# Kernel optimization log

Hardware: AMD Instinct MI355X
Metric: run time of the kernel (lower is better)

## Reference

```python
import jax, jax.numpy as jnp
import numpy as np

N, E, G = 50000, 640000, 512
F_NODE, F_EDGE, HID, H, L = 8, 3, 128, 4, 4
C = HID // H


def setup_inputs() -> dict:
    key = jax.random.key(0)
    ks = jax.random.split(key, 24)
    p = lambda k, s: jax.random.normal(k, s, jnp.float32) * 0.1
    return {
        "x": jax.random.normal(ks[0], (N, F_NODE), jnp.float32),
        "edge_attr": jax.random.normal(ks[1], (E, F_EDGE), jnp.float32),
        "edge_index": jax.random.randint(ks[2], (2, E), 0, N, dtype=jnp.int32),
        "batch": jnp.sort(jax.random.randint(ks[3], (N,), 0, G, dtype=jnp.int32)),
        "enc_node_w": p(ks[4], (F_NODE, HID)), "enc_node_b": p(ks[5], (HID,)),
        "enc_edge_w": p(ks[6], (F_EDGE, HID)), "enc_edge_b": p(ks[7], (HID,)),
        "gat_lin_w": p(ks[8], (L, HID, HID)),
        "gat_att_src": p(ks[9], (L, H, C)),
        "gat_att_dst": p(ks[10], (L, H, C)),
        "gat_lin_edge_w": p(ks[11], (L, HID, HID)),
        "gat_att_edge": p(ks[12], (L, H, C)),
        "gat_bias": p(ks[13], (L, HID)),
        "bn_gamma": jnp.ones((L, HID), jnp.float32),
        "bn_beta": jnp.zeros((L, HID), jnp.float32),
        "fc1_w": p(ks[14], (HID, HID)), "fc1_b": p(ks[15], (HID,)),
        "fc2_w": p(ks[16], (HID, HID // 2)), "fc2_b": p(ks[17], (HID // 2,)),
        "fc3_w": p(ks[18], (HID // 2, 1)), "fc3_b": p(ks[19], (1,)),
    }


def _gat(x, src, dst, ea, lin_w, a_src, a_dst, lin_e_w, a_edge, bias):
    # PyG GATConv (concat=True, negative_slope=0.2, edge_dim=HID)
    xp = (x @ lin_w).reshape(N, H, C)                      # [N,H,C]
    s = jnp.einsum('nhc,hc->nh', xp, a_src)                # alpha_src per node
    d = jnp.einsum('nhc,hc->nh', xp, a_dst)                # alpha_dst per node
    ep = (ea @ lin_e_w).reshape(-1, H, C)                  # [Et,H,C]
    e = jnp.einsum('ehc,hc->eh', ep, a_edge)               # alpha_edge per edge
    alpha = jax.nn.leaky_relu(s[src] + d[dst] + e, 0.2)    # [Et,H]
    # segment softmax over incoming edges of each target node
    m = jax.ops.segment_max(alpha, dst, num_segments=N)
    w = jnp.exp(alpha - m[dst])
    z = jax.ops.segment_sum(w, dst, num_segments=N)
    w = w / (z[dst] + 1e-16)
    msg = xp[src] * w[:, :, None]                          # [Et,H,C]
    out = jax.ops.segment_sum(msg, dst, num_segments=N)
    return out.reshape(N, HID) + bias


def reference(x, edge_attr, edge_index, batch,
              enc_node_w, enc_node_b, enc_edge_w, enc_edge_b,
              gat_lin_w, gat_att_src, gat_att_dst, gat_lin_edge_w, gat_att_edge, gat_bias,
              bn_gamma, bn_beta, fc1_w, fc1_b, fc2_w, fc2_b, fc3_w, fc3_b):
    src, dst = edge_index[0], edge_index[1]
    h = x @ enc_node_w + enc_node_b
    ea = edge_attr @ enc_edge_w + enc_edge_b
    # add_self_loops with fill_value='mean': self-loop attr = mean of incoming edge attrs
    deg = jax.ops.segment_sum(jnp.ones((E,), h.dtype), dst, num_segments=N)
    loop_ea = jax.ops.segment_sum(ea, dst, num_segments=N) / jnp.maximum(deg, 1.0)[:, None]
    loop = jnp.arange(N, dtype=src.dtype)
    src_f = jnp.concatenate([src, loop])
    dst_f = jnp.concatenate([dst, loop])
    ea_f = jnp.concatenate([ea, loop_ea], axis=0)
    for i in range(L):
        hn = _gat(h, src_f, dst_f, ea_f, gat_lin_w[i], gat_att_src[i], gat_att_dst[i],
                  gat_lin_edge_w[i], gat_att_edge[i], gat_bias[i])
        mu = hn.mean(0)
        var = ((hn - mu) ** 2).mean(0)                     # BatchNorm1d training-mode stats
        hn = (hn - mu) / jnp.sqrt(var + 1e-5) * bn_gamma[i] + bn_beta[i]
        hn = jax.nn.relu(hn)
        h = h + hn if i > 0 else hn
    # global mean pool over graphs
    cnt = jax.ops.segment_sum(jnp.ones((N,), h.dtype), batch, num_segments=G)
    g = jax.ops.segment_sum(h, batch, num_segments=G) / jnp.maximum(cnt, 1.0)[:, None]
    g = jax.nn.relu(g @ fc1_w + fc1_b)
    g = jax.nn.relu(g @ fc2_w + fc2_b)
    return g @ fc3_w + fc3_b
```

## Files before the change

kernel.cpp:

```cpp
#include <hip/hip_runtime.h>
#include <hip/hip_bf16.h>

#define NN 50000
#define EE 640000
#define GG 512
#define NPB 16
#define NLB 3125
#define CPX 391
#define CAPD 64
#define CCAP 48
#define WSTR 772
#define PGRP 6250
#define PCH 625
#define PLB8 5000

typedef unsigned int uint;
typedef __attribute__((ext_vector_type(8))) short short8;
typedef __attribute__((ext_vector_type(4))) float floatx4;

__device__ inline float2 bf2f(uint u) {
    return make_float2(__uint_as_float(u << 16), __uint_as_float(u & 0xffff0000u));
}
__device__ inline uint packbf(float a, float b) {
    __hip_bfloat162 t;
    t.x = __float2bfloat16(a);
    t.y = __float2bfloat16(b);
    return *(uint*)&t;
}
__device__ inline uint bfbits(float v) {
    __hip_bfloat16 t = __float2bfloat16(v);
    return (uint)*(unsigned short*)&t;
}
__device__ inline float bflo(uint u) { return __uint_as_float(u << 16); }
__device__ inline float bfhi(uint u) { return __uint_as_float(u & 0xffff0000u); }

__global__ __launch_bounds__(256) void k_prep(const float* __restrict__ lin_e_w,
                                              const float* __restrict__ att_e,
                                              const float* __restrict__ encW,
                                              const float* __restrict__ encB,
                                              const float* __restrict__ W,
                                              const float* __restrict__ x,
                                              const float* __restrict__ nodeW,
                                              const float* __restrict__ nodeB,
                                              const int* __restrict__ src,
                                              const int* __restrict__ dst,
                                              const float* __restrict__ edge_attr,
                                              int* __restrict__ cnt, uint* __restrict__ ed,
                                              float* __restrict__ Mt, float* __restrict__ bns4,
                                              uint* __restrict__ WbT, uint* __restrict__ hb) {
    int tid = threadIdx.x;
    int blk = blockIdx.x;
    if (blk < PLB8) {
        int g = blk & 7;
        int e0 = ((blk >> 3) * 256 + tid) * 4;
        int4 d4 = *(const int4*)(dst + e0);
        int dd[4] = {d4.x, d4.y, d4.z, d4.w};
#pragma unroll
        for (int i = 0; i < 4; i++) {
            if ((unsigned)(dd[i] - g * PGRP) < (unsigned)PGRP) {
                int e = e0 + i;
                int s = src[e];
                const float* ar = edge_attr + (size_t)e * 3;
                uint w0 = (uint)(s & 0xffff) | (bfbits(ar[0]) << 16);
                uint w1 = bfbits(ar[1]) | (bfbits(ar[2]) << 16);
                int p = atomicAdd(&cnt[dd[i]], 1);
                if (p < CAPD)
                    *(uint2*)(ed + ((size_t)dd[i] * CAPD + p) * 2) = make_uint2(w0, w1);
            }
        }
    } else if (blk == PLB8) {
        __shared__ float we[128 * 16];
        for (int idx = tid; idx < 2048; idx += 256) {
            int k = idx >> 4, lh = idx & 15, l = lh >> 2, h = lh & 3;
            const float* wrow = lin_e_w + l * 16384 + k * 128 + h * 32;
            const float* arow = att_e + l * 128 + h * 32;
            float acc = 0.f;
#pragma unroll
            for (int c = 0; c < 32; c++) acc += wrow[c] * arow[c];
            we[k * 16 + lh] = acc;
        }
        for (int i = tid; i < 4 * 8 * 256; i += 256) bns4[i] = 0.f;
        __syncthreads();
        if (tid < 64) {
            int lh = tid >> 2, r = tid & 3;
            float acc = 0.f;
            for (int k = 0; k < 128; k++) {
                float a = (r < 3) ? encW[r * 128 + k] : encB[k];
                acc += a * we[k * 16 + lh];
            }
            Mt[lh * 4 + r] = acc;
        }
    } else if (blk <= PLB8 + 128) {
        int idx = (blk - PLB8 - 1) * 256 + tid;
        int l = idx >> 13, rem = idx & 8191, n = rem >> 6, u = rem & 63;
        const float* Wl = W + l * 16384;
        WbT[idx] = packbf(Wl[(2 * u) * 128 + n], Wl[(2 * u + 1) * 128 + n]);
    } else {
        int idx = (blk - PLB8 - 129) * 256 + tid;
        int n = idx >> 6, c0 = (idx & 63) * 2;
        float a0 = nodeB[c0], a1 = nodeB[c0 + 1];
        const float* xr = x + n * 8;
#pragma unroll
        for (int f = 0; f < 8; f++) {
            a0 += xr[f] * nodeW[f * 128 + c0];
            a1 += xr[f] * nodeW[f * 128 + c0 + 1];
        }
        hb[idx] = packbf(a0, a1);
    }
}

__global__ __launch_bounds__(256) void k_gemm(uint* __restrict__ hb, const uint* __restrict__ gout,
                                              const float* __restrict__ bns,
                                              const float* __restrict__ gamma,
                                              const float* __restrict__ beta,
                                              const uint* __restrict__ WbT,
                                              const float* __restrict__ a_src, const float* __restrict__ a_dst,
                                              uint* __restrict__ xpb, float* __restrict__ s_arr,
                                              float* __restrict__ d_arr, int mode) {
    __shared__ __align__(16) uint Bl[128 * 68];
    __shared__ __align__(16) uint Ah[64 * 66];
    __shared__ float sc[128], sf[128];
    int tid = threadIdx.x;
    int rowBase = blockIdx.x * 64;
    for (int idx = tid; idx < 2048; idx += 256) {
        int n = idx >> 4, u4 = idx & 15;
        uint4 v = *(const uint4*)(WbT + n * 64 + u4 * 4);
        *(uint4*)(&Bl[n * 68 + u4 * 4]) = v;
    }
    if (mode && tid < 128) {
        float s = 0.f, q = 0.f;
#pragma unroll
        for (int k = 0; k < 8; k++) { s += bns[k * 256 + tid]; q += bns[k * 256 + 128 + tid]; }
        float mu = s * (1.f / NN);
        float var = q * (1.f / NN) - mu * mu;
        float iv = rsqrtf(fmaxf(var, 0.f) + 1e-5f);
        float a = gamma[tid] * iv;
        sc[tid] = a;
        sf[tid] = beta[tid] - mu * a;
    }
    __syncthreads();
    if (mode) {
        for (int idx = tid; idx < 4096; idx += 256) {
            int row = idx >> 6, u = idx & 63;
            int gr = rowBase + row;
            uint pk = 0;
            if (gr < NN) {
                float2 v = bf2f(gout[(size_t)gr * 64 + u]);
                int c0 = u * 2;
                float r0 = fmaxf(v.x * sc[c0] + sf[c0], 0.f);
                float r1 = fmaxf(v.y * sc[c0 + 1] + sf[c0 + 1], 0.f);
                if (mode == 2) {
                    float2 hp = bf2f(hb[(size_t)gr * 64 + u]);
                    r0 += hp.x; r1 += hp.y;
                }
                pk = packbf(r0, r1);
                hb[(size_t)gr * 64 + u] = pk;
            }
            Ah[row * 66 + u] = pk;
        }
        __syncthreads();
    }
    int lane = tid & 63, wv = tid >> 6;
    int ln15 = lane & 15, quad = lane >> 4;
    int rowL = wv * 16 + ln15;
    int rowA = rowBase + rowL;
    short8 af[4];
    if (mode) {
#pragma unroll
        for (int c = 0; c < 4; c++)
            af[c] = *(const short8*)((const short*)&Ah[rowL * 66] + c * 32 + quad * 8);
    } else {
        int rowAc = rowA < NN ? rowA : 0;
#pragma unroll
        for (int c = 0; c < 4; c++)
            af[c] = *(const short8*)((const short*)hb + (size_t)rowAc * 128 + c * 32 + quad * 8);
    }
    floatx4 acc[8];
#pragma unroll
    for (int t = 0; t < 8; t++) acc[t] = (floatx4){0.f, 0.f, 0.f, 0.f};
#pragma unroll
    for (int c = 0; c < 4; c++) {
#pragma unroll
        for (int t = 0; t < 8; t++) {
            short8 bf = *(const short8*)((const short*)&Bl[(16 * t + ln15) * 68] + c * 32 + quad * 8);
            acc[t] = __builtin_amdgcn_mfma_f32_16x16x32_bf16(af[c], bf, acc[t], 0, 0, 0);
        }
    }
#pragma unroll
    for (int t = 0; t < 8; t++) {
#pragma unroll
        for (int r = 0; r < 4; r++) {
            float v = acc[t][r];
            float vhi = __shfl_xor(v, 1);
            int grow = rowBase + wv * 16 + quad * 4 + r;
            if (!(ln15 & 1) && grow < NN)
                xpb[(size_t)grow * 64 + 8 * t + (ln15 >> 1)] = packbf(v, vhi);
        }
    }
    float asl[4], ash[4], adl[4], adh[4];
#pragma unroll
    for (int hh = 0; hh < 4; hh++) {
        asl[hh] = a_src[hh * 32 + ln15]; ash[hh] = a_src[hh * 32 + 16 + ln15];
        adl[hh] = a_dst[hh * 32 + ln15]; adh[hh] = a_dst[hh * 32 + 16 + ln15];
    }
#pragma unroll
    for (int r = 0; r < 4; r++) {
        float s0 = acc[0][r] * asl[0] + acc[1][r] * ash[0];
        float s1 = acc[2][r] * asl[1] + acc[3][r] * ash[1];
        float s2 = acc[4][r] * asl[2] + acc[5][r] * ash[2];
        float s3 = acc[6][r] * asl[3] + acc[7][r] * ash[3];
        float d0 = acc[0][r] * adl[0] + acc[1][r] * adh[0];
        float d1 = acc[2][r] * adl[1] + acc[3][r] * adh[1];
        float d2 = acc[4][r] * adl[2] + acc[5][r] * adh[2];
        float d3 = acc[6][r] * adl[3] + acc[7][r] * adh[3];
#pragma unroll
        for (int off = 1; off < 16; off <<= 1) {
            s0 += __shfl_xor(s0, off); s1 += __shfl_xor(s1, off);
            s2 += __shfl_xor(s2, off); s3 += __shfl_xor(s3, off);
            d0 += __shfl_xor(d0, off); d1 += __shfl_xor(d1, off);
            d2 += __shfl_xor(d2, off); d3 += __shfl_xor(d3, off);
        }
        int grow = rowBase + wv * 16 + quad * 4 + r;
        if (ln15 == 0 && grow < NN) {
            *(float4*)(s_arr + grow * 4) = make_float4(s0, s1, s2, s3);
            *(float4*)(d_arr + grow * 4) = make_float4(d0, d1, d2, d3);
        }
    }
}

__global__ __launch_bounds__(256) void k_edge(const int* __restrict__ cnt, const uint* __restrict__ ed,
                                              const float* __restrict__ Mt,
                                              const float* __restrict__ s_arr, const float* __restrict__ d_arr,
                                              const uint* __restrict__ xpb, uint* __restrict__ outb,
                                              float* __restrict__ bns, int layer) {
    __shared__ int kc_sh[NPB];
    __shared__ float d4c[NPB][4];
    __shared__ __align__(16) float shw[4][WSTR];
    __shared__ int shs[NPB * CCAP];
    int tid = threadIdx.x;
    int lb = (blockIdx.x & 7) * CPX + (blockIdx.x >> 3);
    if (lb >= NLB) return;
    int nb0 = lb * NPB;
    if (tid < NPB) {
        int c = cnt[nb0 + tid];
        kc_sh[tid] = c < CAPD ? c : CAPD;
    }
    if (tid < NPB * 4)
        d4c[tid >> 2][tid & 3] = d_arr[(size_t)(nb0 + (tid >> 2)) * 4 + (tid & 3)];
    float4 mt0 = *(const float4*)(Mt + (layer * 4 + 0) * 4);
    float4 mt1 = *(const float4*)(Mt + (layer * 4 + 1) * 4);
    float4 mt2 = *(const float4*)(Mt + (layer * 4 + 2) * 4);
    float4 mt3 = *(const float4*)(Mt + (layer * 4 + 3) * 4);
    __syncthreads();
    {
        int ni = tid >> 4, sub = tid & 15;
        int node = nb0 + ni;
        int k = kc_sh[ni];
        float as0 = 0.f, as1 = 0.f, as2 = 0.f;
        float dv0 = d4c[ni][0], dv1 = d4c[ni][1], dv2 = d4c[ni][2], dv3 = d4c[ni][3];
        for (int j = sub; j < k; j += 16) {
            uint2 r = *(const uint2*)(ed + ((size_t)node * CAPD + j) * 2);
            int sv = r.x & 0xffff;
            float a0 = bfhi(r.x), a1 = bflo(r.y), a2 = bfhi(r.y);
            as0 += a0; as1 += a1; as2 += a2;
            float4 s4 = *(const float4*)(s_arr + (size_t)sv * 4);
            float e_0 = a0 * mt0.x + a1 * mt0.y + a2 * mt0.z + mt0.w;
            float e_1 = a0 * mt1.x + a1 * mt1.y + a2 * mt1.z + mt1.w;
            float e_2 = a0 * mt2.x + a1 * mt2.y + a2 * mt2.z + mt2.w;
            float e_3 = a0 * mt3.x + a1 * mt3.y + a2 * mt3.z + mt3.w;
            float al0 = s4.x + dv0 + e_0; al0 = al0 > 0.f ? al0 : 0.2f * al0;
            float al1 = s4.y + dv1 + e_1; al1 = al1 > 0.f ? al1 : 0.2f * al1;
            float al2 = s4.z + dv2 + e_2; al2 = al2 > 0.f ? al2 : 0.2f * al2;
            float al3 = s4.w + dv3 + e_3; al3 = al3 > 0.f ? al3 : 0.2f * al3;
            if (j < CCAP - 1) {
                int ls = ni * CCAP + 1 + j;
                shs[ls] = sv;
                shw[0][ls] = __expf(al0);
                shw[1][ls] = __expf(al1);
                shw[2][ls] = __expf(al2);
                shw[3][ls] = __expf(al3);
            }
        }
#pragma unroll
        for (int off = 8; off; off >>= 1) {
            as0 += __shfl_xor(as0, off, 16);
            as1 += __shfl_xor(as1, off, 16);
            as2 += __shfl_xor(as2, off, 16);
        }
        if (sub == 0) {
            float inv = 1.f / fmaxf((float)k, 1.f);
            float m0 = as0 * inv, m1 = as1 * inv, m2 = as2 * inv;
            float wf = k > 0 ? 1.f : 0.f;
            float4 sl = *(const float4*)(s_arr + (size_t)node * 4);
            float e_0 = m0 * mt0.x + m1 * mt0.y + m2 * mt0.z + wf * mt0.w;
            float e_1 = m0 * mt1.x + m1 * mt1.y + m2 * mt1.z + wf * mt1.w;
            float e_2 = m0 * mt2.x + m1 * mt2.y + m2 * mt2.z + wf * mt2.w;
            float e_3 = m0 * mt3.x + m1 * mt3.y + m2 * mt3.z + wf * mt3.w;
            float al0 = sl.x + dv0 + e_0; al0 = al0 > 0.f ? al0 : 0.2f * al0;
            float al1 = sl.y + dv1 + e_1; al1 = al1 > 0.f ? al1 : 0.2f * al1;
            float al2 = sl.z + dv2 + e_2; al2 = al2 > 0.f ? al2 : 0.2f * al2;
            float al3 = sl.w + dv3 + e_3; al3 = al3 > 0.f ? al3 : 0.2f * al3;
            int ls = ni * CCAP;
            shs[ls] = node;
            shw[0][ls] = __expf(al0);
            shw[1][ls] = __expf(al1);
            shw[2][ls] = __expf(al2);
            shw[3][ls] = __expf(al3);
        }
    }
    __syncthreads();
    int wv = tid >> 6, lane = tid & 63, hh = lane >> 4;
    float4 mth = hh == 0 ? mt0 : hh == 1 ? mt1 : hh == 2 ? mt2 : mt3;
    float bs0 = 0.f, bs1 = 0.f, bq0 = 0.f, bq1 = 0.f;
#pragma unroll
    for (int q = 0; q < 4; q++) {
        int ni = wv * 4 + q;
        int node = nb0 + ni;
        int k = kc_sh[ni];
        int cached = 1 + (k < CCAP - 1 ? k : CCAP - 1);
        int base = ni * CCAP;
        float acc0 = 0.f, acc1 = 0.f, z = 0.f;
        int j = 0;
        for (; j + 8 <= cached; j += 8) {
            float w[8]; int sv[8]; uint xv[8];
#pragma unroll
            for (int u = 0; u < 8; u++) { w[u] = shw[hh][base + j + u]; sv[u] = shs[base + j + u]; }
#pragma unroll
            for (int u = 0; u < 8; u++) xv[u] = xpb[(size_t)sv[u] * 64 + lane];
#pragma unroll
            for (int u = 0; u < 8; u++) {
                z += w[u];
                float2 f = bf2f(xv[u]);
                acc0 += w[u] * f.x; acc1 += w[u] * f.y;
            }
        }
        for (; j + 4 <= cached; j += 4) {
            float w0 = shw[hh][base + j], w1 = shw[hh][base + j + 1];
            float w2 = shw[hh][base + j + 2], w3 = shw[hh][base + j + 3];
            int s0 = shs[base + j], s1 = shs[base + j + 1];
            int s2 = shs[base + j + 2], s3 = shs[base + j + 3];
            uint x0 = xpb[(size_t)s0 * 64 + lane];
            uint x1 = xpb[(size_t)s1 * 64 + lane];
            uint x2 = xpb[(size_t)s2 * 64 + lane];
            uint x3 = xpb[(size_t)s3 * 64 + lane];
            z += w0 + w1 + w2 + w3;
            float2 f0 = bf2f(x0), f1 = bf2f(x1), f2 = bf2f(x2), f3 = bf2f(x3);
            acc0 += w0 * f0.x + w1 * f1.x + w2 * f2.x + w3 * f3.x;
            acc1 += w0 * f0.y + w1 * f1.y + w2 * f2.y + w3 * f3.y;
        }
        for (; j < cached; j++) {
            float w = shw[hh][base + j];
            int sv = shs[base + j];
            z += w;
            float2 f = bf2f(xpb[(size_t)sv * 64 + lane]);
            acc0 += w * f.x; acc1 += w * f.y;
        }
        for (int je = CCAP - 1; je < k; je++) {
            uint2 r = *(const uint2*)(ed + ((size_t)node * CAPD + je) * 2);
            int sv = r.x & 0xffff;
            float a0 = bfhi(r.x), a1 = bflo(r.y), a2 = bfhi(r.y);
            float sva = s_arr[(size_t)sv * 4 + hh];
            float ev = a0 * mth.x + a1 * mth.y + a2 * mth.z + mth.w;
            float a = sva + d4c[ni][hh] + ev; a = a > 0.f ? a : 0.2f * a;
            float w = __expf(a);
            z += w;
            float2 f = bf2f(xpb[(size_t)sv * 64 + lane]);
            acc0 += w * f.x; acc1 += w * f.y;
        }
        float zi = 1.f / (z + 1e-16f);
        float o0 = acc0 * zi, o1 = acc1 * zi;
        outb[(size_t)node * 64 + lane] = packbf(o0, o1);
        bs0 += o0; bs1 += o1; bq0 += o0 * o0; bq1 += o1 * o1;
    }
    __syncthreads();
    float* scratch = &shw[0][0];
    scratch[wv * 256 + lane * 4 + 0] = bs0;
    scratch[wv * 256 + lane * 4 + 1] = bs1;
    scratch[wv * 256 + lane * 4 + 2] = bq0;
    scratch[wv * 256 + lane * 4 + 3] = bq1;
    __syncthreads();
    float v = scratch[tid] + scratch[256 + tid] + scratch[512 + tid] + scratch[768 + tid];
    int ln = tid >> 2, st = tid & 3;
    int gidx = (st < 2) ? (2 * ln + st) : (128 + 2 * ln + (st - 2));
    atomicAdd(&bns[(blockIdx.x & 7) * 256 + gidx], v);
}

__global__ __launch_bounds__(256) void k_tail(const uint* __restrict__ hb, const uint* __restrict__ gout,
                                              const float* __restrict__ bns,
                                              const float* __restrict__ gamma, const float* __restrict__ beta,
                                              const int* __restrict__ batch,
                                              const float* __restrict__ w1, const float* __restrict__ b1,
                                              const float* __restrict__ w2, const float* __restrict__ b2,
                                              const float* __restrict__ w3, const float* __restrict__ b3,
                                              float* __restrict__ out) {
    __shared__ float sc[128], sf[128];
    __shared__ float sh[2][256];
    __shared__ float gv[128], h1[128], h2[64];
    int tid = threadIdx.x;
    if (tid < 128) {
        float s = 0.f, q = 0.f;
#pragma unroll
        for (int k = 0; k < 8; k++) { s += bns[k * 256 + tid]; q += bns[k * 256 + 128 + tid]; }
        float mu = s * (1.f / NN);
        float var = q * (1.f / NN) - mu * mu;
        float iv = rsqrtf(fmaxf(var, 0.f) + 1e-5f);
        float a = gamma[tid] * iv;
        sc[tid] = a;
        sf[tid] = beta[tid] - mu * a;
    }
    __syncthreads();
    int gi = blockIdx.x;
    int t = tid & 63, rh = tid >> 6;
    int lo = 0, hi = NN;
    while (lo < hi) { int mid = (lo + hi) >> 1; if (batch[mid] < gi) lo = mid + 1; else hi = mid; }
    int start = lo;
    hi = NN;
    while (lo < hi) { int mid = (lo + hi) >> 1; if (batch[mid] < gi + 1) lo = mid + 1; else hi = mid; }
    int end = lo;
    float s0 = 0.f, s1 = 0.f;
    int c0 = t * 2;
    float a0c = sc[c0], a1c = sc[c0 + 1], f0c = sf[c0], f1c = sf[c0 + 1];
    for (int n = start + rh; n < end; n += 4) {
        float2 gvv = bf2f(gout[(size_t)n * 64 + t]);
        float2 hp = bf2f(hb[(size_t)n * 64 + t]);
        s0 += hp.x + fmaxf(gvv.x * a0c + f0c, 0.f);
        s1 += hp.y + fmaxf(gvv.y * a1c + f1c, 0.f);
    }
    sh[0][tid] = s0; sh[1][tid] = s1;
    __syncthreads();
    if (rh == 0) {
        float inv = 1.f / fmaxf((float)(end - start), 1.f);
        gv[2 * t]     = (sh[0][t] + sh[0][64 + t] + sh[0][128 + t] + sh[0][192 + t]) * inv;
        gv[2 * t + 1] = (sh[1][t] + sh[1][64 + t] + sh[1][128 + t] + sh[1][192 + t]) * inv;
    }
    __syncthreads();
    if (tid < 128) {
        float acc = b1[tid];
        for (int kk = 0; kk < 128; kk++) acc += gv[kk] * w1[kk * 128 + tid];
        h1[tid] = fmaxf(acc, 0.f);
    }
    __syncthreads();
    if (tid < 64) {
        float a2 = b2[tid];
        for (int kk = 0; kk < 128; kk++) a2 += h1[kk] * w2[kk * 64 + tid];
        h2[tid] = fmaxf(a2, 0.f);
    }
    __syncthreads();
    if (tid < 64) {
        float p = h2[tid] * w3[tid];
#pragma unroll
        for (int off = 32; off; off >>= 1) p += __shfl_xor(p, off);
        if (tid == 0) out[gi] = p + b3[0];
    }
}

extern "C" void kernel_launch(void* const* d_in, const int* in_sizes, int n_in,
                              void* d_out, int out_size, void* d_ws, size_t ws_size,
                              hipStream_t stream) {
    const float* x            = (const float*)d_in[0];
    const float* edge_attr    = (const float*)d_in[1];
    const int*   edge_index   = (const int*)d_in[2];
    const int*   batch        = (const int*)d_in[3];
    const float* enc_node_w   = (const float*)d_in[4];
    const float* enc_node_b   = (const float*)d_in[5];
    const float* enc_edge_w   = (const float*)d_in[6];
    const float* enc_edge_b   = (const float*)d_in[7];
    const float* gat_lin_w    = (const float*)d_in[8];
    const float* gat_att_src  = (const float*)d_in[9];
    const float* gat_att_dst  = (const float*)d_in[10];
    const float* gat_lin_edge = (const float*)d_in[11];
    const float* gat_att_edge = (const float*)d_in[12];
    const float* bn_gamma     = (const float*)d_in[14];
    const float* bn_beta      = (const float*)d_in[15];
    const float* fc1_w        = (const float*)d_in[16];
    const float* fc1_b        = (const float*)d_in[17];
    const float* fc2_w        = (const float*)d_in[18];
    const float* fc2_b        = (const float*)d_in[19];
    const float* fc3_w        = (const float*)d_in[20];
    const float* fc3_b        = (const float*)d_in[21];
    float* outv = (float*)d_out;

    char* ws = (char*)d_ws;
    size_t off = 0;
    auto alloc = [&](size_t bytes) -> void* {
        void* p = ws + off;
        off = (off + bytes + 255) & ~(size_t)255;
        return p;
    };
    uint*  hbv     = (uint*)alloc((size_t)NN * 64 * 4);
    uint*  goutb   = (uint*)alloc((size_t)NN * 64 * 4);
    uint*  xpb     = (uint*)alloc((size_t)NN * 64 * 4);
    float* s_arr   = (float*)alloc((size_t)NN * 4 * 4);
    float* d_arr   = (float*)alloc((size_t)NN * 4 * 4);
    int*   cnt     = (int*)alloc((size_t)NN * 4);
    uint*  ed      = (uint*)alloc((size_t)NN * CAPD * 8);
    uint*  WbT     = (uint*)alloc((size_t)4 * 128 * 64 * 4);
    float* Mt      = (float*)alloc(64 * 4);
    float* bns4    = (float*)alloc((size_t)4 * 8 * 256 * 4);
    (void)ws_size; (void)in_sizes; (void)n_in; (void)out_size;

    hipMemsetAsync(cnt, 0, NN * 4, stream);

    const int* srce = edge_index;
    const int* dste = edge_index + EE;

    k_prep<<<PLB8 + 129 + (NN * 64) / 256, 256, 0, stream>>>(
        gat_lin_edge, gat_att_edge, enc_edge_w, enc_edge_b, gat_lin_w,
        x, enc_node_w, enc_node_b, srce, dste, edge_attr,
        cnt, ed, Mt, bns4, WbT, hbv);

    int gemmBlocks = (NN + 63) / 64;
    for (int l = 0; l < 4; l++) {
        int mode = (l == 0) ? 0 : (l == 1 ? 1 : 2);
        const float* bnsPrev = bns4 + (l - 1) * 2048;
        k_gemm<<<gemmBlocks, 256, 0, stream>>>(hbv, goutb,
                                               mode ? bnsPrev : bns4,
                                               bn_gamma + (l ? (l - 1) * 128 : 0),
                                               bn_beta + (l ? (l - 1) * 128 : 0),
                                               WbT + l * 8192,
                                               gat_att_src + l * 128, gat_att_dst + l * 128,
                                               xpb, s_arr, d_arr, mode);
        k_edge<<<8 * CPX, 256, 0, stream>>>(cnt, ed, Mt, s_arr, d_arr, xpb, goutb,
                                            bns4 + l * 2048, l);
    }

    k_tail<<<GG, 256, 0, stream>>>(hbv, goutb, bns4 + 3 * 2048, bn_gamma + 3 * 128,
                                   bn_beta + 3 * 128, batch,
                                   fc1_w, fc1_b, fc2_w, fc2_b, fc3_w, fc3_b, outv);
}
```

Measured before the change: 424.5 us.

## Two-pass bucketed CSR build replacing per-node global atomics in edge prep

Result: slower. 446.0 us (+5.1%).

```diff
diff --git a/kernel.cpp b/kernel.cpp
--- a/kernel.cpp
+++ b/kernel.cpp
@@ -7,12 +7,12 @@
 #define NPB 16
 #define NLB 3125
 #define CPX 391
-#define CAPD 64
+#define CAPD 48
 #define CCAP 48
 #define WSTR 772
-#define PGRP 6250
-#define PCH 625
-#define PLB8 5000
+#define NBKT 391
+#define BCAP 512
+#define PLA 625
 
 typedef unsigned int uint;
 typedef __attribute__((ext_vector_type(8))) short short8;
@@ -45,30 +45,34 @@
                                               const int* __restrict__ src,
                                               const int* __restrict__ dst,
                                               const float* __restrict__ edge_attr,
-                                              int* __restrict__ cnt, uint* __restrict__ ed,
+                                              int* __restrict__ bcnt, uint* __restrict__ bkt,
                                               float* __restrict__ Mt, float* __restrict__ bns4,
                                               uint* __restrict__ WbT, uint* __restrict__ hb) {
     int tid = threadIdx.x;
     int blk = blockIdx.x;
-    if (blk < PLB8) {
-        int g = blk & 7;
-        int e0 = ((blk >> 3) * 256 + tid) * 4;
+    if (blk < PLA) {
+        int inst = blk & 7;
+        int e0 = (blk * 256 + tid) * 4;
         int4 d4 = *(const int4*)(dst + e0);
+        int4 s4 = *(const int4*)(src + e0);
+        const float4* ar4 = (const float4*)(edge_attr + (size_t)e0 * 3);
+        float4 q0 = ar4[0], q1 = ar4[1], q2 = ar4[2];
+        const float* a = &q0.x;
         int dd[4] = {d4.x, d4.y, d4.z, d4.w};
+        int ss[4] = {s4.x, s4.y, s4.z, s4.w};
 #pragma unroll
         for (int i = 0; i < 4; i++) {
-            if ((unsigned)(dd[i] - g * PGRP) < (unsigned)PGRP) {
-                int e = e0 + i;
-                int s = src[e];
-                const float* ar = edge_attr + (size_t)e * 3;
-                uint w0 = (uint)(s & 0xffff) | (bfbits(ar[0]) << 16);
-                uint w1 = bfbits(ar[1]) | (bfbits(ar[2]) << 16);
-                int p = atomicAdd(&cnt[dd[i]], 1);
-                if (p < CAPD)
-                    *(uint2*)(ed + ((size_t)dd[i] * CAPD + p) * 2) = make_uint2(w0, w1);
-            }
-        }
-    } else if (blk == PLB8) {
+            int d = dd[i];
+            int b = d >> 7;
+            uint w0 = (uint)(ss[i] & 0xffff) | ((uint)(d & 127) << 16);
+            uint w1 = bfbits(a[3 * i]) | (bfbits(a[3 * i + 1]) << 16);
+            uint w2 = bfbits(a[3 * i + 2]);
+            int p = atomicAdd(&bcnt[inst * NBKT + b], 1);
+            if (p < BCAP)
+                *(uint4*)(bkt + ((size_t)(inst * NBKT + b) * BCAP + p) * 4) =
+                    make_uint4(w0, w1, w2, 0u);
+        }
+    } else if (blk == PLA) {
         __shared__ float we[128 * 16];
         for (int idx = tid; idx < 2048; idx += 256) {
             int k = idx >> 4, lh = idx & 15, l = lh >> 2, h = lh & 3;
@@ -90,13 +94,13 @@
             }
             Mt[lh * 4 + r] = acc;
         }
-    } else if (blk <= PLB8 + 128) {
-        int idx = (blk - PLB8 - 1) * 256 + tid;
+    } else if (blk <= PLA + 128) {
+        int idx = (blk - PLA - 1) * 256 + tid;
         int l = idx >> 13, rem = idx & 8191, n = rem >> 6, u = rem & 63;
         const float* Wl = W + l * 16384;
         WbT[idx] = packbf(Wl[(2 * u) * 128 + n], Wl[(2 * u + 1) * 128 + n]);
     } else {
-        int idx = (blk - PLB8 - 129) * 256 + tid;
+        int idx = (blk - PLA - 129) * 256 + tid;
         int n = idx >> 6, c0 = (idx & 63) * 2;
         float a0 = nodeB[c0], a1 = nodeB[c0 + 1];
         const float* xr = x + n * 8;
@@ -107,6 +111,37 @@
         }
         hb[idx] = packbf(a0, a1);
     }
+}
+
+__global__ __launch_bounds__(256) void k_place2(const int* __restrict__ bcnt,
+                                                const uint* __restrict__ bkt,
+                                                uint* __restrict__ ed, int* __restrict__ cnt) {
+    __shared__ uint2 slots[128 * CAPD];
+    __shared__ int lcnt[128];
+    int tid = threadIdx.x, b = blockIdx.x;
+    int node0 = b * 128;
+    int nInB = NN - node0; if (nInB > 128) nInB = 128;
+    if (tid < 128) lcnt[tid] = 0;
+    __syncthreads();
+#pragma unroll 1
+    for (int j = 0; j < 8; j++) {
+        int n = bcnt[j * NBKT + b]; if (n > BCAP) n = BCAP;
+        const uint* base = bkt + (size_t)(j * NBKT + b) * BCAP * 4;
+        for (int i = tid; i < n; i += 256) {
+            uint4 r = *(const uint4*)(base + (size_t)i * 4);
+            int dstl = (r.x >> 16) & 127;
+            int p = atomicAdd(&lcnt[dstl], 1);
+            if (p < CAPD)
+                slots[dstl * CAPD + p] = make_uint2((r.x & 0xffffu) | (r.y << 16),
+                                                    (r.y >> 16) | (r.z << 16));
+        }
+    }
+    __syncthreads();
+    int total = nInB * CAPD;
+    uint* d0 = ed + (size_t)node0 * CAPD * 2;
+    for (int idx = tid; idx < total; idx += 256)
+        *(uint2*)(d0 + (size_t)idx * 2) = slots[idx];
+    if (tid < nInB) cnt[node0 + tid] = lcnt[tid];
 }
 
 __global__ __launch_bounds__(256) void k_gemm(uint* __restrict__ hb, const uint* __restrict__ gout,
@@ -494,20 +529,23 @@
     float* d_arr   = (float*)alloc((size_t)NN * 4 * 4);
     int*   cnt     = (int*)alloc((size_t)NN * 4);
     uint*  ed      = (uint*)alloc((size_t)NN * CAPD * 8);
+    int*   bcnt    = (int*)alloc((size_t)8 * NBKT * 4);
+    uint*  bkt     = (uint*)alloc((size_t)8 * NBKT * BCAP * 16);
     uint*  WbT     = (uint*)alloc((size_t)4 * 128 * 64 * 4);
     float* Mt      = (float*)alloc(64 * 4);
     float* bns4    = (float*)alloc((size_t)4 * 8 * 256 * 4);
     (void)ws_size; (void)in_sizes; (void)n_in; (void)out_size;
 
-    hipMemsetAsync(cnt, 0, NN * 4, stream);
+    hipMemsetAsync(bcnt, 0, (size_t)8 * NBKT * 4, stream);
 
     const int* srce = edge_index;
     const int* dste = edge_index + EE;
 
-    k_prep<<<PLB8 + 129 + (NN * 64) / 256, 256, 0, stream>>>(
+    k_prep<<<PLA + 129 + (NN * 64) / 256, 256, 0, stream>>>(
         gat_lin_edge, gat_att_edge, enc_edge_w, enc_edge_b, gat_lin_w,
         x, enc_node_w, enc_node_b, srce, dste, edge_attr,
-        cnt, ed, Mt, bns4, WbT, hbv);
+        bcnt, bkt, Mt, bns4, WbT, hbv);
+    k_place2<<<NBKT, 256, 0, stream>>>(bcnt, bkt, ed, cnt);
 
     int gemmBlocks = (NN + 63) / 64;
     for (int l = 0; l < 4; l++) {
```
